# Performance work log

Hardware: AMD Instinct MI355X
Metric: run time of the kernel (lower is better)

The kernel has to match this reference:

```python
import jax, jax.numpy as jnp
import numpy as np

B, S, H, F, E, TOP_K = 2, 1024, 2048, 1408, 8, 2
SHARED_F = 2 * F  # moe_intermediate_size * n_shared_experts


def setup_inputs() -> dict:
    key = jax.random.key(0)
    ks = jax.random.split(key, 8)
    s = 0.02  # init scale for weights
    return {
        "hidden_states": jax.random.normal(ks[0], (B, S, H), jnp.float32),
        "gate_weight": jax.random.normal(ks[1], (E, H), jnp.float32) * s,
        "gate_proj": jax.random.normal(ks[2], (E, H, F), jnp.float32) * s,
        "up_proj": jax.random.normal(ks[3], (E, H, F), jnp.float32) * s,
        "down_proj": jax.random.normal(ks[4], (E, F, H), jnp.float32) * s,
        "shared_gate": jax.random.normal(ks[5], (H, SHARED_F), jnp.float32) * s,
        "shared_up": jax.random.normal(ks[6], (H, SHARED_F), jnp.float32) * s,
        "shared_down": jax.random.normal(ks[7], (SHARED_F, H), jnp.float32) * s,
    }


def reference(hidden_states, gate_weight, gate_proj, up_proj, down_proj,
              shared_gate, shared_up, shared_down):
    orig_shape = hidden_states.shape
    x = hidden_states.reshape(-1, orig_shape[-1])  # [T, H]
    T = x.shape[0]

    # MoEGate: softmax scores, top-k routing (no renorm)
    scores = jax.nn.softmax(x @ gate_weight.T, axis=-1)  # [T, E]
    topk_w, topk_idx = jax.lax.top_k(scores, TOP_K)      # [T, K]
    # dense combine weights: zero except selected experts
    combine = jnp.zeros_like(scores).at[jnp.arange(T)[:, None], topk_idx].set(topk_w)  # [T, E]

    # FusedSigmaMLP on all experts (math equal to sort/pad/grouped-GEMM/scatter-add path)
    gate_h = jnp.einsum('td,edf->etf', x, gate_proj)     # [E, T, F]
    up_h = jnp.einsum('td,edf->etf', x, up_proj)          # [E, T, F]
    expert_out = jnp.einsum('etf,efd->etd', jax.nn.silu(gate_h) * up_h, down_proj)  # [E, T, H]
    y = jnp.einsum('etd,te->td', expert_out, combine)     # weighted combine

    # shared experts (SigmaMLP with intermediate = moe_intermediate * n_shared)
    shared = (jax.nn.silu(x @ shared_gate) * (x @ shared_up)) @ shared_down
    return (y + shared).reshape(orig_shape)
```

## Files before the change

kernel.cpp:

```cpp
#include <hip/hip_runtime.h>
#include <hip/hip_bf16.h>

constexpr int T_ = 2048;
constexpr int H_ = 2048;
constexpr int F_ = 1408;
constexpr int E_ = 8;
constexpr int SF_ = 2816;

typedef __bf16 bf16;
typedef bf16 bf16x8 __attribute__((ext_vector_type(8)));
typedef float f32x4 __attribute__((ext_vector_type(4)));

#define DEVI __device__ __forceinline__

DEVI void async16(const void* g, void* l) {
    __builtin_amdgcn_global_load_lds(
        (const __attribute__((address_space(1))) unsigned int*)g,
        (__attribute__((address_space(3))) unsigned int*)l, 16, 0, 0);
}

__global__ void transpose_cvt(const float* __restrict__ src, bf16* __restrict__ dst,
                              int R, int C) {
    int z = blockIdx.z;
    src += (size_t)z * R * C;
    dst += (size_t)z * R * C;
    __shared__ float tile[32][33];
    int tx = threadIdx.x, ty = threadIdx.y;
    int c0 = blockIdx.x * 32, r0 = blockIdx.y * 32;
#pragma unroll
    for (int i = 0; i < 4; i++)
        tile[ty + i * 8][tx] = src[(size_t)(r0 + ty + i * 8) * C + c0 + tx];
    __syncthreads();
#pragma unroll
    for (int i = 0; i < 4; i++)
        dst[(size_t)(c0 + ty + i * 8) * R + r0 + tx] = (bf16)tile[tx][ty + i * 8];
}

__global__ void convert_x(const float* __restrict__ x, bf16* __restrict__ xb) {
    int i = (blockIdx.x * 256 + threadIdx.x) * 8;
    float4 a = *(const float4*)(x + i);
    float4 b = *(const float4*)(x + i + 4);
    bf16x8 v;
    v[0] = (bf16)a.x; v[1] = (bf16)a.y; v[2] = (bf16)a.z; v[3] = (bf16)a.w;
    v[4] = (bf16)b.x; v[5] = (bf16)b.y; v[6] = (bf16)b.z; v[7] = (bf16)b.w;
    *(bf16x8*)(xb + i) = v;
}

__global__ void gate_route(const float* __restrict__ x, const float* __restrict__ gw,
                           int* __restrict__ cnt, int* __restrict__ list,
                           float* __restrict__ wlist) {
    int t = blockIdx.x;
    int tid = threadIdx.x;
    float p[E_];
#pragma unroll
    for (int e = 0; e < E_; e++) p[e] = 0.f;
    const float* xr = x + (size_t)t * H_;
    for (int h = tid; h < H_; h += 256) {
        float xv = xr[h];
#pragma unroll
        for (int e = 0; e < E_; e++) p[e] += xv * gw[e * H_ + h];
    }
#pragma unroll
    for (int e = 0; e < E_; e++)
#pragma unroll
        for (int off = 32; off > 0; off >>= 1) p[e] += __shfl_down(p[e], off, 64);
    __shared__ float wred[4][E_];
    int lane = tid & 63, wid = tid >> 6;
    if (lane == 0)
#pragma unroll
        for (int e = 0; e < E_; e++) wred[wid][e] = p[e];
    __syncthreads();
    if (tid == 0) {
        float l[E_];
#pragma unroll
        for (int e = 0; e < E_; e++) l[e] = wred[0][e] + wred[1][e] + wred[2][e] + wred[3][e];
        float mx = l[0];
#pragma unroll
        for (int e = 1; e < E_; e++) mx = fmaxf(mx, l[e]);
        float sc[E_], s = 0.f;
#pragma unroll
        for (int e = 0; e < E_; e++) { sc[e] = __expf(l[e] - mx); s += sc[e]; }
#pragma unroll
        for (int e = 0; e < E_; e++) sc[e] /= s;
        int i1 = 0;
#pragma unroll
        for (int e = 1; e < E_; e++) if (sc[e] > sc[i1]) i1 = e;
        int i2 = (i1 == 0) ? 1 : 0;
#pragma unroll
        for (int e = 0; e < E_; e++) if (e != i1 && sc[e] > sc[i2]) i2 = e;
        int p1 = atomicAdd(&cnt[i1], 1);
        list[i1 * T_ + p1] = t; wlist[i1 * T_ + p1] = sc[i1];
        int p2 = atomicAdd(&cnt[i2], 1);
        list[i2 * T_ + p2] = t; wlist[i2 * T_ + p2] = sc[i2];
    }
}

__global__ void gather_rows(const bf16* __restrict__ xb, const int* __restrict__ cnt,
                            const int* __restrict__ list, bf16* __restrict__ xA) {
    int i = blockIdx.x, e = blockIdx.y;
    if (i >= cnt[e]) return;
    int t = list[e * T_ + i];
    const float4* s = (const float4*)(xb + (size_t)t * H_);
    float4* d = (float4*)(xA + ((size_t)e * T_ + i) * H_);
    d[threadIdx.x] = s[threadIdx.x];
}

__global__ void gemm_dual(const bf16* __restrict__ A, const bf16* __restrict__ Bg,
                          const bf16* __restrict__ Bu, bf16* __restrict__ Cact,
                          const int* __restrict__ cntPtr, int Mfull, int K, int N,
                          long sAe, long sBe, long sCe) {
    int e = blockIdx.z;
    A += (size_t)e * sAe; Bg += (size_t)e * sBe; Bu += (size_t)e * sBe;
    Cact += (size_t)e * sCe;
    int M = cntPtr ? cntPtr[e] : Mfull;
    int row0 = blockIdx.y * 128;
    if (row0 >= M) return;
    int col0 = blockIdx.x * 64;

    __shared__ __align__(16) bf16 As[128 * 64];
    __shared__ __align__(16) bf16 Bgs[64 * 64];
    __shared__ __align__(16) bf16 Bus[64 * 64];

    int tid = threadIdx.x, lane = tid & 63, wid = tid >> 6;
    int wm = (wid >> 1) * 64, wn = (wid & 1) * 32;
    int lm = lane & 15, lq = lane >> 4;

    f32x4 accg[4][2] = {};
    f32x4 accu[4][2] = {};

    int nkt = K >> 6;
    for (int kt = 0; kt < nkt; kt++) {
        int k0 = kt * 64;
#pragma unroll
        for (int j = 0; j < 4; j++) {
            int L = j * 256 + tid;
            int m = L >> 3, cp = L & 7, c = cp ^ (m & 7);
            int gr = row0 + m; if (gr >= M) gr = M - 1;
            async16(A + (size_t)gr * K + k0 + c * 8, (void*)(As + L * 8));
        }
#pragma unroll
        for (int j = 0; j < 2; j++) {
            int L = j * 256 + tid;
            int n = L >> 3, cp = L & 7, c = cp ^ (n & 7);
            async16(Bg + (size_t)(col0 + n) * K + k0 + c * 8, (void*)(Bgs + L * 8));
            async16(Bu + (size_t)(col0 + n) * K + k0 + c * 8, (void*)(Bus + L * 8));
        }
        __syncthreads();
#pragma unroll
        for (int kk = 0; kk < 2; kk++) {
            bf16x8 af[4], bgf[2], buf_[2];
            int cc = kk * 4 + lq;
#pragma unroll
            for (int mi = 0; mi < 4; mi++) {
                int r = wm + mi * 16 + lm;
                af[mi] = *(const bf16x8*)(As + r * 64 + ((cc ^ (r & 7)) * 8));
            }
#pragma unroll
            for (int ni = 0; ni < 2; ni++) {
                int r = wn + ni * 16 + lm;
                bgf[ni]  = *(const bf16x8*)(Bgs + r * 64 + ((cc ^ (r & 7)) * 8));
                buf_[ni] = *(const bf16x8*)(Bus + r * 64 + ((cc ^ (r & 7)) * 8));
            }
#pragma unroll
            for (int mi = 0; mi < 4; mi++)
#pragma unroll
                for (int ni = 0; ni < 2; ni++) {
                    accg[mi][ni] = __builtin_amdgcn_mfma_f32_16x16x32_bf16(af[mi], bgf[ni], accg[mi][ni], 0, 0, 0);
                    accu[mi][ni] = __builtin_amdgcn_mfma_f32_16x16x32_bf16(af[mi], buf_[ni], accu[mi][ni], 0, 0, 0);
                }
        }
        __syncthreads();
    }
#pragma unroll
    for (int mi = 0; mi < 4; mi++)
#pragma unroll
        for (int r = 0; r < 4; r++) {
            int gr = row0 + wm + mi * 16 + lq * 4 + r;
            if (gr >= M) continue;
#pragma unroll
            for (int ni = 0; ni < 2; ni++) {
                int gc = col0 + wn + ni * 16 + lm;
                float g = accg[mi][ni][r], u = accu[mi][ni][r];
                float act = g / (1.f + __expf(-g)) * u;
                Cact[(size_t)gr * N + gc] = (bf16)act;
            }
        }
}

__global__ void gemm_single(const bf16* __restrict__ A, const bf16* __restrict__ Bt,
                            float* __restrict__ Out, const int* __restrict__ cntPtr,
                            int Mfull, int K, int N, const int* __restrict__ list,
                            const float* __restrict__ wlist, long sAe, long sBe) {
    int e = blockIdx.z;
    A += (size_t)e * sAe; Bt += (size_t)e * sBe;
    const int* lst = list ? list + (size_t)e * T_ : nullptr;
    const float* wl = wlist ? wlist + (size_t)e * T_ : nullptr;
    int M = cntPtr ? cntPtr[e] : Mfull;
    int row0 = blockIdx.y * 128;
    if (row0 >= M) return;
    int col0 = blockIdx.x * 128;

    __shared__ __align__(16) bf16 As[128 * 64];
    __shared__ __align__(16) bf16 Bs[128 * 64];

    int tid = threadIdx.x, lane = tid & 63, wid = tid >> 6;
    int wm = (wid >> 1) * 64, wn = (wid & 1) * 64;
    int lm = lane & 15, lq = lane >> 4;

    f32x4 acc[4][4] = {};
    int nkt = K >> 6;
    for (int kt = 0; kt < nkt; kt++) {
        int k0 = kt * 64;
#pragma unroll
        for (int j = 0; j < 4; j++) {
            int L = j * 256 + tid;
            int m = L >> 3, cp = L & 7, c = cp ^ (m & 7);
            int gr = row0 + m; if (gr >= M) gr = M - 1;
            async16(A + (size_t)gr * K + k0 + c * 8, (void*)(As + L * 8));
            async16(Bt + (size_t)(col0 + m) * K + k0 + c * 8, (void*)(Bs + L * 8));
        }
        __syncthreads();
#pragma unroll
        for (int kk = 0; kk < 2; kk++) {
            bf16x8 af[4], bfr[4];
            int cc = kk * 4 + lq;
#pragma unroll
            for (int i = 0; i < 4; i++) {
                int ra = wm + i * 16 + lm;
                af[i] = *(const bf16x8*)(As + ra * 64 + ((cc ^ (ra & 7)) * 8));
                int rb = wn + i * 16 + lm;
                bfr[i] = *(const bf16x8*)(Bs + rb * 64 + ((cc ^ (rb & 7)) * 8));
            }
#pragma unroll
            for (int mi = 0; mi < 4; mi++)
#pragma unroll
                for (int ni = 0; ni < 4; ni++)
                    acc[mi][ni] = __builtin_amdgcn_mfma_f32_16x16x32_bf16(af[mi], bfr[ni], acc[mi][ni], 0, 0, 0);
        }
        __syncthreads();
    }
#pragma unroll
    for (int mi = 0; mi < 4; mi++)
#pragma unroll
        for (int r = 0; r < 4; r++) {
            int cr = row0 + wm + mi * 16 + lq * 4 + r;
            if (cr >= M) continue;
            if (lst) {
                int t = lst[cr];
                float w = wl[cr];
#pragma unroll
                for (int ni = 0; ni < 4; ni++) {
                    int gc = col0 + wn + ni * 16 + lm;
                    atomicAdd(&Out[(size_t)t * N + gc], w * acc[mi][ni][r]);
                }
            } else {
#pragma unroll
                for (int ni = 0; ni < 4; ni++) {
                    int gc = col0 + wn + ni * 16 + lm;
                    Out[(size_t)cr * N + gc] = acc[mi][ni][r];
                }
            }
        }
}

extern "C" void kernel_launch(void* const* d_in, const int* in_sizes, int n_in,
                              void* d_out, int out_size, void* d_ws, size_t ws_size,
                              hipStream_t stream) {
    const float* x     = (const float*)d_in[0];
    const float* gw    = (const float*)d_in[1];
    const float* gproj = (const float*)d_in[2];
    const float* uproj = (const float*)d_in[3];
    const float* dproj = (const float*)d_in[4];
    const float* sg    = (const float*)d_in[5];
    const float* su    = (const float*)d_in[6];
    const float* sd    = (const float*)d_in[7];
    float* out = (float*)d_out;

    char* w = (char*)d_ws;
    size_t off = 0;
    auto alloc = [&](size_t bytes) { void* p = w + off; off += (bytes + 255) & ~(size_t)255; return p; };
    bf16* wg_t   = (bf16*)alloc((size_t)E_ * F_ * H_ * 2);
    bf16* wu_t   = (bf16*)alloc((size_t)E_ * F_ * H_ * 2);
    bf16* wd_t   = (bf16*)alloc((size_t)E_ * H_ * F_ * 2);
    bf16* sg_t   = (bf16*)alloc((size_t)SF_ * H_ * 2);
    bf16* su_t   = (bf16*)alloc((size_t)SF_ * H_ * 2);
    bf16* sd_t   = (bf16*)alloc((size_t)H_ * SF_ * 2);
    bf16* xb     = (bf16*)alloc((size_t)T_ * H_ * 2);
    bf16* xA     = (bf16*)alloc((size_t)E_ * T_ * H_ * 2);
    bf16* act    = (bf16*)alloc((size_t)E_ * T_ * F_ * 2);
    bf16* act_sh = (bf16*)alloc((size_t)T_ * SF_ * 2);
    int*  cnt    = (int*)alloc(256);
    int*  list   = (int*)alloc((size_t)E_ * T_ * 4);
    float* wlist = (float*)alloc((size_t)E_ * T_ * 4);
    (void)ws_size; (void)in_sizes; (void)n_in; (void)out_size;

    hipMemsetAsync(cnt, 0, 256, stream);

    dim3 tb(32, 8);
    transpose_cvt<<<dim3(F_ / 32, H_ / 32, E_), tb, 0, stream>>>(gproj, wg_t, H_, F_);
    transpose_cvt<<<dim3(F_ / 32, H_ / 32, E_), tb, 0, stream>>>(uproj, wu_t, H_, F_);
    transpose_cvt<<<dim3(H_ / 32, F_ / 32, E_), tb, 0, stream>>>(dproj, wd_t, F_, H_);
    transpose_cvt<<<dim3(SF_ / 32, H_ / 32, 1), tb, 0, stream>>>(sg, sg_t, H_, SF_);
    transpose_cvt<<<dim3(SF_ / 32, H_ / 32, 1), tb, 0, stream>>>(su, su_t, H_, SF_);
    transpose_cvt<<<dim3(H_ / 32, SF_ / 32, 1), tb, 0, stream>>>(sd, sd_t, SF_, H_);

    convert_x<<<T_ * H_ / (256 * 8), 256, 0, stream>>>(x, xb);
    gate_route<<<T_, 256, 0, stream>>>(x, gw, cnt, list, wlist);
    gather_rows<<<dim3(T_, E_), 256, 0, stream>>>(xb, cnt, list, xA);

    gemm_dual<<<dim3(F_ / 64, T_ / 128, E_), 256, 0, stream>>>(
        xA, wg_t, wu_t, act, cnt, T_, H_, F_,
        (long)T_ * H_, (long)F_ * H_, (long)T_ * F_);
    gemm_dual<<<dim3(SF_ / 64, T_ / 128, 1), 256, 0, stream>>>(
        xb, sg_t, su_t, act_sh, nullptr, T_, H_, SF_, 0, 0, 0);
    gemm_single<<<dim3(H_ / 128, T_ / 128, 1), 256, 0, stream>>>(
        act_sh, sd_t, out, nullptr, T_, SF_, H_, nullptr, nullptr, 0, 0);
    gemm_single<<<dim3(H_ / 128, T_ / 128, E_), 256, 0, stream>>>(
        act, wd_t, out, cnt, T_, F_, H_, list, wlist,
        (long)T_ * F_, (long)H_ * F_);
}
```

Baseline: 678.7 us.

## Fuse transposes, gate/convert, and merge shared+expert GEMMs into single launches

Combines the six weight transpose launches into one kernel with 64x64 tiles, vectorized float4 loads and bf16x8 stores. Fuses the x conversion into the gating kernel. Merges the shared and routed gate/up GEMMs into one grid, and the shared and routed down GEMMs into another. The launch order is swizzled so blocks that share a weight slab run close together. The routing weight moves into the activation epilogue, and the shared down-projection is split over K with atomic accumulation into a zeroed output. This adds a memset, turns the shared output into atomics, and rounds the combine weight to bf16 earlier.

```diff
diff --git a/kernel.cpp b/kernel.cpp
--- a/kernel.cpp
+++ b/kernel.cpp
@@ -13,53 +13,81 @@
 
 #define DEVI __device__ __forceinline__
 
+constexpr int GU_SH = 768;
+constexpr int GU_EX = 3072;
+constexpr int GU_GRID = GU_SH + GU_EX;
+constexpr int DN_SH = 512;
+constexpr int DN_EX = 2048;
+constexpr int DN_GRID = DN_SH + DN_EX;
+
 DEVI void async16(const void* g, void* l) {
     __builtin_amdgcn_global_load_lds(
         (const __attribute__((address_space(1))) unsigned int*)g,
         (__attribute__((address_space(3))) unsigned int*)l, 16, 0, 0);
 }
 
-__global__ void transpose_cvt(const float* __restrict__ src, bf16* __restrict__ dst,
-                              int R, int C) {
-    int z = blockIdx.z;
-    src += (size_t)z * R * C;
-    dst += (size_t)z * R * C;
-    __shared__ float tile[32][33];
-    int tx = threadIdx.x, ty = threadIdx.y;
-    int c0 = blockIdx.x * 32, r0 = blockIdx.y * 32;
-#pragma unroll
-    for (int i = 0; i < 4; i++)
-        tile[ty + i * 8][tx] = src[(size_t)(r0 + ty + i * 8) * C + c0 + tx];
+__global__ void mega_transpose(const float* __restrict__ gp, const float* __restrict__ up,
+                               const float* __restrict__ dp, const float* __restrict__ sg,
+                               const float* __restrict__ su, const float* __restrict__ sd,
+                               bf16* __restrict__ wg, bf16* __restrict__ wu,
+                               bf16* __restrict__ wd, bf16* __restrict__ sgt,
+                               bf16* __restrict__ sut, bf16* __restrict__ sdt) {
+    int id = blockIdx.x;
+    const float* src; bf16* dst; int R, C, t;
+    if (id < 5632)       { int e = id / 704; t = id % 704; R = 2048; C = 1408;
+                           src = gp + (size_t)e * R * C; dst = wg + (size_t)e * R * C; }
+    else if (id < 11264) { int e = (id - 5632) / 704; t = (id - 5632) % 704; R = 2048; C = 1408;
+                           src = up + (size_t)e * R * C; dst = wu + (size_t)e * R * C; }
+    else if (id < 16896) { int e = (id - 11264) / 704; t = (id - 11264) % 704; R = 1408; C = 2048;
+                           src = dp + (size_t)e * R * C; dst = wd + (size_t)e * R * C; }
+    else if (id < 18304) { t = id - 16896; R = 2048; C = 2816; src = sg; dst = sgt; }
+    else if (id < 19712) { t = id - 18304; R = 2048; C = 2816; src = su; dst = sut; }
+    else                 { t = id - 19712; R = 2816; C = 2048; src = sd; dst = sdt; }
+    int tiles_c = C >> 6;
+    int r0 = (t / tiles_c) * 64, c0 = (t % tiles_c) * 64;
+
+    __shared__ float tile[64][68];
+    int th = threadIdx.x;
+    int lr = th >> 4, lc4 = (th & 15) * 4;
+#pragma unroll
+    for (int i = 0; i < 4; i++) {
+        int r = lr + i * 16;
+        float4 v = *(const float4*)(src + (size_t)(r0 + r) * C + c0 + lc4);
+        *(float4*)&tile[r][lc4] = v;
+    }
     __syncthreads();
 #pragma unroll
-    for (int i = 0; i < 4; i++)
-        dst[(size_t)(c0 + ty + i * 8) * R + r0 + tx] = (bf16)tile[tx][ty + i * 8];
-}
-
-__global__ void convert_x(const float* __restrict__ x, bf16* __restrict__ xb) {
-    int i = (blockIdx.x * 256 + threadIdx.x) * 8;
-    float4 a = *(const float4*)(x + i);
-    float4 b = *(const float4*)(x + i + 4);
+    for (int p = 0; p < 2; p++) {
+        int ch = th + p * 256;
+        int c = ch & 63, rq = ch >> 6;
+        bf16x8 o;
+#pragma unroll
+        for (int j = 0; j < 8; j++) o[j] = (bf16)tile[rq * 8 + j][c];
+        *(bf16x8*)(dst + (size_t)(c0 + c) * R + r0 + rq * 8) = o;
+    }
+}
+
+__global__ void gate_cvt_route(const float* __restrict__ x, const float* __restrict__ gw,
+                               bf16* __restrict__ xb, int* __restrict__ cnt,
+                               int* __restrict__ list, float* __restrict__ wlist) {
+    int t = blockIdx.x, tid = threadIdx.x;
+    const float* xr = x + (size_t)t * H_;
+    int h0 = tid * 8;
+    float4 a = *(const float4*)(xr + h0);
+    float4 b = *(const float4*)(xr + h0 + 4);
+    float xv[8] = {a.x, a.y, a.z, a.w, b.x, b.y, b.z, b.w};
     bf16x8 v;
-    v[0] = (bf16)a.x; v[1] = (bf16)a.y; v[2] = (bf16)a.z; v[3] = (bf16)a.w;
-    v[4] = (bf16)b.x; v[5] = (bf16)b.y; v[6] = (bf16)b.z; v[7] = (bf16)b.w;
-    *(bf16x8*)(xb + i) = v;
-}
-
-__global__ void gate_route(const float* __restrict__ x, const float* __restrict__ gw,
-                           int* __restrict__ cnt, int* __restrict__ list,
-                           float* __restrict__ wlist) {
-    int t = blockIdx.x;
-    int tid = threadIdx.x;
+#pragma unroll
+    for (int j = 0; j < 8; j++) v[j] = (bf16)xv[j];
+    *(bf16x8*)(xb + (size_t)t * H_ + h0) = v;
+
     float p[E_];
 #pragma unroll
     for (int e = 0; e < E_; e++) p[e] = 0.f;
-    const float* xr = x + (size_t)t * H_;
-    for (int h = tid; h < H_; h += 256) {
-        float xv = xr[h];
-#pragma unroll
-        for (int e = 0; e < E_; e++) p[e] += xv * gw[e * H_ + h];
-    }
+#pragma unroll
+    for (int j = 0; j < 8; j++)
+#pragma unroll
+        for (int e = 0; e < E_; e++) p[e] += xv[j] * gw[e * H_ + h0 + j];
 #pragma unroll
     for (int e = 0; e < E_; e++)
 #pragma unroll
@@ -105,17 +133,37 @@
     d[threadIdx.x] = s[threadIdx.x];
 }
 
-__global__ void gemm_dual(const bf16* __restrict__ A, const bf16* __restrict__ Bg,
-                          const bf16* __restrict__ Bu, bf16* __restrict__ Cact,
-                          const int* __restrict__ cntPtr, int Mfull, int K, int N,
-                          long sAe, long sBe, long sCe) {
-    int e = blockIdx.z;
-    A += (size_t)e * sAe; Bg += (size_t)e * sBe; Bu += (size_t)e * sBe;
-    Cact += (size_t)e * sCe;
-    int M = cntPtr ? cntPtr[e] : Mfull;
-    int row0 = blockIdx.y * 128;
-    if (row0 >= M) return;
-    int col0 = blockIdx.x * 64;
+__global__ void gemm_gu(const bf16* __restrict__ xb, const bf16* __restrict__ xA,
+                        const bf16* __restrict__ sgt, const bf16* __restrict__ sut,
+                        const bf16* __restrict__ wg, const bf16* __restrict__ wu,
+                        bf16* __restrict__ act_sh, bf16* __restrict__ act,
+                        const int* __restrict__ cnt, const float* __restrict__ wlist) {
+    int id = blockIdx.x;
+    const bf16 *A, *Bg, *Bu; bf16* C;
+    const float* wl = nullptr;
+    int M, N, row0, col0;
+    if (id < GU_SH) {
+        int x = id & 7, u = id >> 3;
+        int cg = u >> 4, rb = u & 15;
+        int col = cg * 8 + x;
+        if (col >= 44) return;
+        A = xb; Bg = sgt; Bu = sut; C = act_sh;
+        M = T_; N = SF_; row0 = rb * 128; col0 = col * 64;
+    } else {
+        int id2 = id - GU_SH;
+        int x = id2 & 7, u = id2 >> 3;
+        int e = u / 48, t2 = u % 48, j = t2 >> 4, rb = t2 & 15;
+        int col = ((x - e) & 7) + 8 * j;
+        if (col >= 22) return;
+        M = cnt[e]; row0 = rb * 128;
+        if (row0 >= M) return;
+        A = xA + (size_t)e * T_ * H_;
+        Bg = wg + (size_t)e * F_ * H_;
+        Bu = wu + (size_t)e * F_ * H_;
+        C = act + (size_t)e * T_ * F_;
+        wl = wlist + (size_t)e * T_;
+        N = F_; col0 = col * 64;
+    }
 
     __shared__ __align__(16) bf16 As[128 * 64];
     __shared__ __align__(16) bf16 Bgs[64 * 64];
@@ -127,8 +175,8 @@
 
     f32x4 accg[4][2] = {};
     f32x4 accu[4][2] = {};
-
-    int nkt = K >> 6;
+    constexpr int nkt = H_ >> 6;
+
     for (int kt = 0; kt < nkt; kt++) {
         int k0 = kt * 64;
 #pragma unroll
@@ -136,14 +184,14 @@
             int L = j * 256 + tid;
             int m = L >> 3, cp = L & 7, c = cp ^ (m & 7);
             int gr = row0 + m; if (gr >= M) gr = M - 1;
-            async16(A + (size_t)gr * K + k0 + c * 8, (void*)(As + L * 8));
+            async16(A + (size_t)gr * H_ + k0 + c * 8, (void*)(As + L * 8));
         }
 #pragma unroll
         for (int j = 0; j < 2; j++) {
             int L = j * 256 + tid;
             int n = L >> 3, cp = L & 7, c = cp ^ (n & 7);
-            async16(Bg + (size_t)(col0 + n) * K + k0 + c * 8, (void*)(Bgs + L * 8));
-            async16(Bu + (size_t)(col0 + n) * K + k0 + c * 8, (void*)(Bus + L * 8));
+            async16(Bg + (size_t)(col0 + n) * H_ + k0 + c * 8, (void*)(Bgs + L * 8));
+            async16(Bu + (size_t)(col0 + n) * H_ + k0 + c * 8, (void*)(Bus + L * 8));
         }
         __syncthreads();
 #pragma unroll
@@ -177,28 +225,42 @@
         for (int r = 0; r < 4; r++) {
             int gr = row0 + wm + mi * 16 + lq * 4 + r;
             if (gr >= M) continue;
+            float wv = wl ? wl[gr] : 1.f;
 #pragma unroll
             for (int ni = 0; ni < 2; ni++) {
                 int gc = col0 + wn + ni * 16 + lm;
                 float g = accg[mi][ni][r], u = accu[mi][ni][r];
-                float act = g / (1.f + __expf(-g)) * u;
-                Cact[(size_t)gr * N + gc] = (bf16)act;
-            }
-        }
-}
-
-__global__ void gemm_single(const bf16* __restrict__ A, const bf16* __restrict__ Bt,
-                            float* __restrict__ Out, const int* __restrict__ cntPtr,
-                            int Mfull, int K, int N, const int* __restrict__ list,
-                            const float* __restrict__ wlist, long sAe, long sBe) {
-    int e = blockIdx.z;
-    A += (size_t)e * sAe; Bt += (size_t)e * sBe;
-    const int* lst = list ? list + (size_t)e * T_ : nullptr;
-    const float* wl = wlist ? wlist + (size_t)e * T_ : nullptr;
-    int M = cntPtr ? cntPtr[e] : Mfull;
-    int row0 = blockIdx.y * 128;
-    if (row0 >= M) return;
-    int col0 = blockIdx.x * 128;
+                float actv = wv * (g / (1.f + __expf(-g)) * u);
+                C[(size_t)gr * N + gc] = (bf16)actv;
+            }
+        }
+}
+
+__global__ void gemm_down(const bf16* __restrict__ act_sh, const bf16* __restrict__ sdt,
+                          const bf16* __restrict__ act, const bf16* __restrict__ wd,
+                          float* __restrict__ out, const int* __restrict__ cnt,
+                          const int* __restrict__ list) {
+    int id = blockIdx.x;
+    const bf16 *A, *B; const int* lst = nullptr;
+    int M, KA, kbase, row0, col0;
+    if (id < DN_SH) {
+        int x = id & 7, u = id >> 3;
+        int cg = u >> 5, rest = u & 31, rb = rest >> 1, ks = rest & 1;
+        int col = cg * 8 + x;
+        A = act_sh; B = sdt; M = T_; KA = SF_; kbase = ks * 1408;
+        row0 = rb * 128; col0 = col * 128;
+    } else {
+        int id2 = id - DN_SH;
+        int x = id2 & 7, u = id2 >> 3;
+        int e = u >> 5, t2 = u & 31, j = t2 >> 4, rb = t2 & 15;
+        int col = ((x - e) & 7) + 8 * j;
+        M = cnt[e]; row0 = rb * 128;
+        if (row0 >= M) return;
+        A = act + (size_t)e * T_ * F_;
+        B = wd + (size_t)e * H_ * F_;
+        lst = list + (size_t)e * T_;
+        KA = F_; kbase = 0; col0 = col * 128;
+    }
 
     __shared__ __align__(16) bf16 As[128 * 64];
     __shared__ __align__(16) bf16 Bs[128 * 64];
@@ -208,16 +270,17 @@
     int lm = lane & 15, lq = lane >> 4;
 
     f32x4 acc[4][4] = {};
-    int nkt = K >> 6;
+    constexpr int nkt = 1408 >> 6;
+
     for (int kt = 0; kt < nkt; kt++) {
-        int k0 = kt * 64;
+        int k0 = kbase + kt * 64;
 #pragma unroll
         for (int j = 0; j < 4; j++) {
             int L = j * 256 + tid;
             int m = L >> 3, cp = L & 7, c = cp ^ (m & 7);
             int gr = row0 + m; if (gr >= M) gr = M - 1;
-            async16(A + (size_t)gr * K + k0 + c * 8, (void*)(As + L * 8));
-            async16(Bt + (size_t)(col0 + m) * K + k0 + c * 8, (void*)(Bs + L * 8));
+            async16(A + (size_t)gr * KA + k0 + c * 8, (void*)(As + L * 8));
+            async16(B + (size_t)(col0 + m) * KA + k0 + c * 8, (void*)(Bs + L * 8));
         }
         __syncthreads();
 #pragma unroll
@@ -228,8 +291,8 @@
             for (int i = 0; i < 4; i++) {
                 int ra = wm + i * 16 + lm;
                 af[i] = *(const bf16x8*)(As + ra * 64 + ((cc ^ (ra & 7)) * 8));
-                int rb = wn + i * 16 + lm;
-                bfr[i] = *(const bf16x8*)(Bs + rb * 64 + ((cc ^ (rb & 7)) * 8));
+                int rb2 = wn + i * 16 + lm;
+                bfr[i] = *(const bf16x8*)(Bs + rb2 * 64 + ((cc ^ (rb2 & 7)) * 8));
             }
 #pragma unroll
             for (int mi = 0; mi < 4; mi++)
@@ -245,20 +308,11 @@
         for (int r = 0; r < 4; r++) {
             int cr = row0 + wm + mi * 16 + lq * 4 + r;
             if (cr >= M) continue;
-            if (lst) {
-                int t = lst[cr];
-                float w = wl[cr];
-#pragma unroll
-                for (int ni = 0; ni < 4; ni++) {
-                    int gc = col0 + wn + ni * 16 + lm;
-                    atomicAdd(&Out[(size_t)t * N + gc], w * acc[mi][ni][r]);
-                }
-            } else {
-#pragma unroll
-                for (int ni = 0; ni < 4; ni++) {
-                    int gc = col0 + wn + ni * 16 + lm;
-                    Out[(size_t)cr * N + gc] = acc[mi][ni][r];
-                }
+            int t = lst ? lst[cr] : cr;
+#pragma unroll
+            for (int ni = 0; ni < 4; ni++) {
+                int gc = col0 + wn + ni * 16 + lm;
+                atomicAdd(&out[(size_t)t * H_ + gc], acc[mi][ni][r]);
             }
         }
 }
@@ -295,27 +349,14 @@
     (void)ws_size; (void)in_sizes; (void)n_in; (void)out_size;
 
     hipMemsetAsync(cnt, 0, 256, stream);
-
-    dim3 tb(32, 8);
-    transpose_cvt<<<dim3(F_ / 32, H_ / 32, E_), tb, 0, stream>>>(gproj, wg_t, H_, F_);
-    transpose_cvt<<<dim3(F_ / 32, H_ / 32, E_), tb, 0, stream>>>(uproj, wu_t, H_, F_);
-    transpose_cvt<<<dim3(H_ / 32, F_ / 32, E_), tb, 0, stream>>>(dproj, wd_t, F_, H_);
-    transpose_cvt<<<dim3(SF_ / 32, H_ / 32, 1), tb, 0, stream>>>(sg, sg_t, H_, SF_);
-    transpose_cvt<<<dim3(SF_ / 32, H_ / 32, 1), tb, 0, stream>>>(su, su_t, H_, SF_);
-    transpose_cvt<<<dim3(H_ / 32, SF_ / 32, 1), tb, 0, stream>>>(sd, sd_t, SF_, H_);
-
-    convert_x<<<T_ * H_ / (256 * 8), 256, 0, stream>>>(x, xb);
-    gate_route<<<T_, 256, 0, stream>>>(x, gw, cnt, list, wlist);
+    hipMemsetAsync(out, 0, (size_t)T_ * H_ * 4, stream);
+
+    mega_transpose<<<21120, 256, 0, stream>>>(gproj, uproj, dproj, sg, su, sd,
+                                              wg_t, wu_t, wd_t, sg_t, su_t, sd_t);
+    gate_cvt_route<<<T_, 256, 0, stream>>>(x, gw, xb, cnt, list, wlist);
     gather_rows<<<dim3(T_, E_), 256, 0, stream>>>(xb, cnt, list, xA);
 
-    gemm_dual<<<dim3(F_ / 64, T_ / 128, E_), 256, 0, stream>>>(
-        xA, wg_t, wu_t, act, cnt, T_, H_, F_,
-        (long)T_ * H_, (long)F_ * H_, (long)T_ * F_);
-    gemm_dual<<<dim3(SF_ / 64, T_ / 128, 1), 256, 0, stream>>>(
-        xb, sg_t, su_t, act_sh, nullptr, T_, H_, SF_, 0, 0, 0);
-    gemm_single<<<dim3(H_ / 128, T_ / 128, 1), 256, 0, stream>>>(
-        act_sh, sd_t, out, nullptr, T_, SF_, H_, nullptr, nullptr, 0, 0);
-    gemm_single<<<dim3(H_ / 128, T_ / 128, E_), 256, 0, stream>>>(
-        act, wd_t, out, cnt, T_, F_, H_, list, wlist,
-        (long)T_ * F_, (long)H_ * F_);
-}
+    gemm_gu<<<GU_GRID, 256, 0, stream>>>(xb, xA, sg_t, su_t, wg_t, wu_t,
+                                         act_sh, act, cnt, wlist);
+    gemm_down<<<DN_GRID, 256, 0, stream>>>(act_sh, sd_t, act, wd_t, out, cnt, list);
+}
```

Result: faster. 637.1 us (-6.1%).
